# Kernel tuning notes

Measured on AMD Instinct MI355X. Metric: run time of the kernel, lower is better.

Reference implementation:

```python
import jax, jax.numpy as jnp
import numpy as np

B, A, C_CLS = 64, 9, 20
H_FEAT, W_FEAT = 28, 28
IN_DIM, HID = 1280, 128
N_GT, M_POS = 40, 2048
AC5 = 5 * A + C_CLS


def setup_inputs() -> dict:
    key = jax.random.key(0)
    ks = jax.random.split(key, 10)
    features = jax.random.normal(ks[0], (B, IN_DIM, H_FEAT, W_FEAT), jnp.float32)
    # valid GT boxes in feature-map coordinates: (x1, y1, x2, y2, class)
    x1 = jax.random.uniform(ks[1], (B, N_GT), minval=0.0, maxval=W_FEAT - 6.0)
    y1 = jax.random.uniform(ks[2], (B, N_GT), minval=0.0, maxval=H_FEAT - 6.0)
    bw = jax.random.uniform(ks[3], (B, N_GT), minval=1.0, maxval=5.0)
    bh = jax.random.uniform(ks[4], (B, N_GT), minval=1.0, maxval=5.0)
    cls = jax.random.randint(ks[5], (B, N_GT), 0, C_CLS).astype(jnp.float32)
    bboxes = jnp.stack([x1, y1, x1 + bw, y1 + bh, cls], axis=-1)
    n_anchors_total = B * A * H_FEAT * W_FEAT
    pos_anchor_idx = jax.random.randint(ks[6], (M_POS,), 0, n_anchors_total, dtype=jnp.int32)
    neg_anchor_idx = jax.random.randint(ks[7], (M_POS,), 0, n_anchors_total, dtype=jnp.int32)
    W1 = jax.random.normal(ks[8], (HID, IN_DIM), jnp.float32) * 0.02
    b1 = jnp.zeros((HID,), jnp.float32)
    W2 = jax.random.normal(ks[9], (AC5, HID), jnp.float32) * 0.02
    b2 = jnp.zeros((AC5,), jnp.float32)
    anc = jnp.array([[1.0, 1], [2, 2], [3, 3], [4, 4], [5, 5], [2, 3], [3, 2], [3, 5], [5, 3]], jnp.float32)
    return dict(features=features, bboxes=bboxes, pos_anchor_idx=pos_anchor_idx,
                neg_anchor_idx=neg_anchor_idx, W1=W1, b1=b1, W2=W2, b2=b2, anc=anc)


def _detector_loss(features, bboxes, pos_idx, neg_idx, W1, b1, W2, b2, anc):
    Bx, _, Hf, Wf = features.shape
    N = bboxes.shape[1]
    Mp = pos_idx.shape[0]
    # ---- prediction network: two 1x1 convs (dropout skipped: eval mode) ----
    h = jnp.einsum('bchw,oc->bohw', features, W1) + b1[None, :, None, None]
    h = jax.nn.leaky_relu(h, 0.01)
    x = jnp.einsum('bchw,oc->bohw', h, W2) + b2[None, :, None, None]
    x_anchor = x[:, :5 * A].reshape(Bx, A, 5, Hf, Wf)  # (B,A,5,H,W)
    x_class = x[:, 5 * A:]                              # (B,C,H,W)
    # ---- GenerateGrid + GenerateAnchor ----
    xs = jnp.arange(Wf, dtype=jnp.float32) + 0.5
    ys = jnp.arange(Hf, dtype=jnp.float32) + 0.5
    gx, gy = jnp.meshgrid(xs, ys, indexing='xy')        # both (H,W)
    grid = jnp.stack([gx, gy], axis=-1)                 # (H,W,2)
    half = anc / 2.0                                    # (A,2)
    tl = grid[None] - half[:, None, None]               # (A,H,W,2)
    br = grid[None] + half[:, None, None]
    anchors = jnp.concatenate([tl, br], axis=-1)        # (A,H,W,4)
    p = jnp.broadcast_to(anchors[None], (Bx, A, Hf, Wf, 4)).reshape(Bx, -1, 4)  # (B,M,4)
    # ---- IoU matrix (B, M, N), exactly as source (signed w*h -> positive area) ----
    area_p = ((p[..., 0] - p[..., 2]) * (p[..., 1] - p[..., 3]))[:, :, None]
    area_b = ((bboxes[..., 2] - bboxes[..., 0]) * (bboxes[..., 3] - bboxes[..., 1]))[:, None, :]
    ix1 = jnp.maximum(p[:, :, None, 0], bboxes[:, None, :, 0])
    iy1 = jnp.maximum(p[:, :, None, 1], bboxes[:, None, :, 1])
    ix2 = jnp.minimum(p[:, :, None, 2], bboxes[:, None, :, 2])
    iy2 = jnp.minimum(p[:, :, None, 3], bboxes[:, None, :, 3])
    inter = jnp.clip(ix2 - ix1, 0.0) * jnp.clip(iy2 - iy1, 0.0)
    iou_mat = inter / (area_p + area_b - inter)          # (B,M,N)
    # ---- gather-based anchor/class extraction ----
    anc_data = jnp.transpose(x_anchor, (0, 1, 3, 4, 2)).reshape(-1, 5)  # (B*A*H*W, 5)
    pos_a = anc_data[pos_idx]
    neg_a = anc_data[neg_idx]
    conf_scores = jax.nn.sigmoid(jnp.concatenate([pos_a[:, 0], neg_a[:, 0]])[:, None])  # (2M,1)
    off = pos_a[:, 1:]
    offsets = jnp.concatenate([jax.nn.sigmoid(off[:, :2]) - 0.5, off[:, 2:]], axis=1)   # (M,4)
    cls_all = jnp.transpose(x_class, (0, 2, 3, 1))                       # (B,H,W,C)
    cls_all = jnp.broadcast_to(cls_all[:, None], (Bx, A, Hf, Wf, C_CLS)).reshape(-1, C_CLS)
    class_scores = cls_all[pos_idx]                                      # (M,C)
    # ---- match positives to GT via IoU argmax, build GT offsets/classes ----
    Mflat = A * Hf * Wf
    bpos = pos_idx // Mflat
    mpos = pos_idx % Mflat
    iou_pos = iou_mat[bpos, mpos]                 # (M,N)
    matched = jnp.argmax(iou_pos, axis=1)         # (M,)
    gt_box = bboxes[bpos, matched]                # (M,5)
    a_box = p[bpos, mpos]                         # (M,4)
    xa = 0.5 * (a_box[:, 0] + a_box[:, 2]); ya = 0.5 * (a_box[:, 1] + a_box[:, 3])
    wa = a_box[:, 2] - a_box[:, 0];          ha = a_box[:, 3] - a_box[:, 1]
    xb = 0.5 * (gt_box[:, 0] + gt_box[:, 2]); yb = 0.5 * (gt_box[:, 1] + gt_box[:, 3])
    wb = gt_box[:, 2] - gt_box[:, 0];          hb = gt_box[:, 3] - gt_box[:, 1]
    gt_offsets = jnp.stack([xb - xa, yb - ya, jnp.log(wb / wa), jnp.log(hb / ha)], axis=1)
    gt_offsets = jax.lax.stop_gradient(gt_offsets)
    gt_cls = gt_box[:, 4].astype(jnp.int32)
    # ---- losses (w_conf = w_reg = w_cls = 1) ----
    gt_conf = jnp.concatenate([jnp.ones((Mp, 1), jnp.float32), jnp.zeros((Mp, 1), jnp.float32)], axis=0)
    conf_loss = jnp.sum((conf_scores - gt_conf) ** 2) / (2.0 * Mp)
    reg_loss = jnp.sum((offsets - gt_offsets) ** 2) / Mp
    logp = jax.nn.log_softmax(class_scores, axis=-1)
    cls_loss = -jnp.mean(jnp.take_along_axis(logp, gt_cls[:, None], axis=1))
    return conf_loss + reg_loss + cls_loss


def reference(features, bboxes, pos_anchor_idx, neg_anchor_idx, W1, b1, W2, b2, anc):
    return _detector_loss(features, bboxes, pos_anchor_idx, neg_anchor_idx, W1, b1, W2, b2, anc)
```

## Files before the change

kernel.cpp:

```cpp
#include <hip/hip_runtime.h>
#include <math.h>

#define NPOS   2048
#define NANCH  4096
#define CIN    1280
#define HID    128
#define W_     28
#define HW_    784
#define AHW    7056
#define FB     (CIN*HW_)
#define SLAB   4
#define SLABF  (SLAB*HW_)

__device__ __forceinline__ float sigmoidf_(float x) {
    return 1.0f / (1.0f + __expf(-x));
}
__device__ __forceinline__ unsigned short f2bf(float x) {
    unsigned int u = __float_as_uint(x);
    return (unsigned short)((u + 0x7fffu + ((u >> 16) & 1u)) >> 16);
}
__device__ __forceinline__ float bf_lo(unsigned int w) { return __uint_as_float(w << 16); }
__device__ __forceinline__ float bf_hi(unsigned int w) { return __uint_as_float(w & 0xffff0000u); }

typedef __attribute__((address_space(3))) float lds_f;
typedef __attribute__((address_space(1))) const float glb_f;
__device__ __forceinline__ void gload16(const float* g, float* l) {
    __builtin_amdgcn_global_load_lds((glb_f*)g, (lds_f*)l, 16, 0, 0);
}

#define SCHED_FENCE() __builtin_amdgcn_sched_barrier(0)
#define WAIT_VM4()  asm volatile("s_waitcnt vmcnt(4)" ::: "memory")
#define WAIT_VM3()  asm volatile("s_waitcnt vmcnt(3)" ::: "memory")
#define WAIT_VM0()  asm volatile("s_waitcnt vmcnt(0)" ::: "memory")
#define WAIT_LGKM0() asm volatile("s_waitcnt lgkmcnt(0)" ::: "memory")

__global__ __launch_bounds__(256, 4) void k_fused(
    const float* __restrict__ F, const float* __restrict__ W1,
    const int* __restrict__ posi, const int* __restrict__ negi,
    unsigned short* __restrict__ Hp, int kchunk, int nslab)
{
    __shared__ float Pl[2][SLABF];
    __shared__ float Wl[2][520];
    __shared__ int   pkl[128];
    __shared__ int   nbL;

    const int b    = blockIdx.x;
    const int ks   = blockIdx.y;
    const int t    = threadIdx.x;
    const int w    = t >> 6;
    const int lane = t & 63;

    if (t == 0) nbL = 0;
    if (t < 128) pkl[t] = 0;
    __syncthreads();

    const int kb0 = ks * kchunk;

    auto issue = [&](int sl2, int buf) {
        const int kb = kb0 + sl2 * SLAB;
        const float* srcP = F + (size_t)b * FB + (size_t)kb * HW_;
        float* dstP = &Pl[buf][0];
#pragma unroll
        for (int i = 0; i < 3; ++i) {
            const int c = w + 4 * i;
            gload16(srcP + c * 256 + lane * 4, dstP + c * 256);
        }
        if (w == 3) {
            if (lane < 16) gload16(srcP + 3072 + lane * 4, dstP + 3072);
        }
        if (w == 1) gload16(W1 + (size_t)lane * CIN + kb, &Wl[buf][0]);
        if (w == 2) gload16(W1 + (size_t)(64 + lane) * CIN + kb, &Wl[buf][260]);
    };

    issue(0, 0);
    issue(1, 1);

#pragma unroll
    for (int r = 0; r < 16; ++r) {
        const int g    = r * 256 + t;
        const int aidx = (g < NPOS) ? posi[g] : negi[g - NPOS];
        const int bb   = aidx / AHW;
        if (bb == b) {
            const int hw   = (aidx - bb * AHW) % HW_;
            const int slot = atomicAdd(&nbL, 1);
            if (slot < 128) pkl[slot] = (g << 10) | hw;
        }
    }
    WAIT_LGKM0();
    SCHED_FENCE();
    __builtin_amdgcn_s_barrier();
    SCHED_FENCE();

    const int  nb   = nbL;
    const bool wact = (w * 32) < nb;
    const int  og   = lane >> 3;
    const int  al   = w * 32 + (lane & 7) * 4;
    int hwr[4], gr[4];
#pragma unroll
    for (int ai = 0; ai < 4; ++ai) {
        const int a  = al + ai;
        const int pk = pkl[a];
        hwr[ai] = pk & 1023;
        gr[ai]  = (a < nb) ? (pk >> 10) : -1;
    }
    const int WB = (og < 4) ? og * 64 : 260 + (og - 4) * 64;

    float acc[4][16];
#pragma unroll
    for (int ai = 0; ai < 4; ++ai)
#pragma unroll
        for (int m = 0; m < 16; ++m) acc[ai][m] = 0.0f;

    if (w == 0) { WAIT_VM3(); } else { WAIT_VM4(); }
    SCHED_FENCE();
    __builtin_amdgcn_s_barrier();
    SCHED_FENCE();

    for (int sl = 0; sl < nslab; ++sl) {
        const int cur = sl & 1;
        if (wact) {
            float ga[4][4];
#pragma unroll
            for (int ai = 0; ai < 4; ++ai)
#pragma unroll
                for (int c = 0; c < 4; ++c)
                    ga[ai][c] = Pl[cur][c * HW_ + hwr[ai]];
#pragma unroll
            for (int m = 0; m < 16; ++m) {
                const float4 wv = *(const float4*)&Wl[cur][WB + 4 * m];
#pragma unroll
                for (int ai = 0; ai < 4; ++ai) {
                    float v = acc[ai][m];
                    v = fmaf(ga[ai][0], wv.x, v);
                    v = fmaf(ga[ai][1], wv.y, v);
                    v = fmaf(ga[ai][2], wv.z, v);
                    v = fmaf(ga[ai][3], wv.w, v);
                    acc[ai][m] = v;
                }
            }
        }
        if (sl + 1 < nslab) {
            WAIT_LGKM0();
            SCHED_FENCE();
            __builtin_amdgcn_s_barrier();
            SCHED_FENCE();
            if (sl + 2 < nslab) {
                issue(sl + 2, cur);
                SCHED_FENCE();
                if (w == 0) { WAIT_VM3(); } else { WAIT_VM4(); }
            } else {
                WAIT_VM0();
            }
            SCHED_FENCE();
            __builtin_amdgcn_s_barrier();
            SCHED_FENCE();
        }
    }

    if (wact) {
#pragma unroll
        for (int ai = 0; ai < 4; ++ai) {
            const int g = gr[ai];
            if (g >= 0) {
                unsigned short* dst =
                    Hp + ((size_t)ks * NANCH + g) * HID + og * 16;
                unsigned u[8];
#pragma unroll
                for (int q = 0; q < 8; ++q)
                    u[q] = (unsigned)f2bf(acc[ai][2 * q]) |
                           ((unsigned)f2bf(acc[ai][2 * q + 1]) << 16);
                *(uint4*)(dst)     = make_uint4(u[0], u[1], u[2], u[3]);
                *(uint4*)(dst + 8) = make_uint4(u[4], u[5], u[6], u[7]);
            }
        }
    }
}

__global__ __launch_bounds__(256) void k_loss(
    const unsigned short* __restrict__ Hp, const float* __restrict__ b1,
    int ksel, const float* __restrict__ W2, const float* __restrict__ b2,
    const int* __restrict__ posi, const int* __restrict__ negi,
    const float* __restrict__ bboxes, const float* __restrict__ anc,
    float* __restrict__ contrib)
{
    const int wid  = threadIdx.x >> 6;
    const int lane = threadIdx.x & 63;
    const int g    = blockIdx.x * 4 + wid;

    const int aidx = (g < NPOS) ? posi[g] : negi[g - NPOS];
    const int b   = aidx / AHW;
    const int rem = aidx - b * AHW;
    const int a   = rem / HW_;
    const int hw  = rem - a * HW_;
    const int hh  = hw / W_;
    const int ww  = hw - hh * W_;

    float hx = b1[2 * lane], hy = b1[2 * lane + 1];
    for (int ks = 0; ks < ksel; ++ks) {
        const unsigned raw =
            *(const unsigned*)&Hp[((size_t)ks * NANCH + g) * HID + 2 * lane];
        hx += bf_lo(raw);
        hy += bf_hi(raw);
    }
    hx = (hx > 0.0f) ? hx : 0.01f * hx;
    hy = (hy > 0.0f) ? hy : 0.01f * hy;

    if (g < NPOS) {
        float outv[25];
#pragma unroll
        for (int j = 0; j < 25; ++j) {
            const int row = (j < 5) ? (5 * a + j) : (40 + j);
            const float2 w = *(const float2*)&W2[(size_t)row * HID + 2 * lane];
            float v = fmaf(w.x, hx, w.y * hy);
#pragma unroll
            for (int off = 1; off < 64; off <<= 1) v += __shfl_xor(v, off, 64);
            outv[j] = v + b2[row];
        }

        const float wa = anc[2 * a], ha = anc[2 * a + 1];
        const float cx = ww + 0.5f, cy = hh + 0.5f;
        const float ax1 = cx - 0.5f * wa, ay1 = cy - 0.5f * ha;
        const float ax2 = cx + 0.5f * wa, ay2 = cy + 0.5f * ha;
        const float areap = wa * ha;

        float v; int vi = lane;
        if (lane < 40) {
            const float* bb = &bboxes[(size_t)(b * 40 + lane) * 5];
            const float bx1 = bb[0], by1 = bb[1], bx2 = bb[2], by2 = bb[3];
            const float areab = (bx2 - bx1) * (by2 - by1);
            const float ix1 = fmaxf(ax1, bx1), iy1 = fmaxf(ay1, by1);
            const float ix2 = fminf(ax2, bx2), iy2 = fminf(ay2, by2);
            const float inter = fmaxf(ix2 - ix1, 0.0f) * fmaxf(iy2 - iy1, 0.0f);
            v = inter / (areap + areab - inter);
        } else {
            v = -1.0f;
        }
#pragma unroll
        for (int off = 1; off < 64; off <<= 1) {
            const float ov = __shfl_xor(v, off, 64);
            const int   oi = __shfl_xor(vi, off, 64);
            if (ov > v || (ov == v && oi < vi)) { v = ov; vi = oi; }
        }
        const int m = vi;

        const float* gt = &bboxes[(size_t)(b * 40 + m) * 5];
        const float gx1 = gt[0], gy1 = gt[1], gx2 = gt[2], gy2 = gt[3];
        const int   gcls = (int)gt[4];
        const float xb = 0.5f * (gx1 + gx2), yb = 0.5f * (gy1 + gy2);
        const float wb = gx2 - gx1, hb = gy2 - gy1;
        const float go0 = xb - cx, go1 = yb - cy;
        const float go2 = __logf(wb / wa), go3 = __logf(hb / ha);

        const float o0 = sigmoidf_(outv[1]) - 0.5f;
        const float o1 = sigmoidf_(outv[2]) - 0.5f;
        const float o2 = outv[3], o3 = outv[4];
        const float reg = (o0 - go0) * (o0 - go0) + (o1 - go1) * (o1 - go1) +
                          (o2 - go2) * (o2 - go2) + (o3 - go3) * (o3 - go3);

        const float conf = sigmoidf_(outv[0]);
        const float conft = (conf - 1.0f) * (conf - 1.0f);

        float mx = outv[5];
#pragma unroll
        for (int c = 1; c < 20; ++c) mx = fmaxf(mx, outv[5 + c]);
        float se = 0.0f;
#pragma unroll
        for (int c = 0; c < 20; ++c) se += __expf(outv[5 + c] - mx);
        float lgt = 0.0f;
#pragma unroll
        for (int c = 0; c < 20; ++c) if (c == gcls) lgt = outv[5 + c];
        const float clst = -(lgt - mx - __logf(se));

        if (lane == 0)
            contrib[g] = conft * (1.0f / 4096.0f) + reg * (1.0f / 2048.0f) +
                         clst * (1.0f / 2048.0f);
    } else {
        const int row = 5 * a;
        const float2 w = *(const float2*)&W2[(size_t)row * HID + 2 * lane];
        float v = fmaf(w.x, hx, w.y * hy);
#pragma unroll
        for (int off = 1; off < 64; off <<= 1) v += __shfl_xor(v, off, 64);
        const float conf = sigmoidf_(v + b2[row]);
        if (lane == 0) contrib[g] = conf * conf * (1.0f / 4096.0f);
    }
}

__global__ __launch_bounds__(256) void k_final(const float* __restrict__ contrib,
                                               float* __restrict__ out)
{
    __shared__ float red[256];
    const int t = threadIdx.x;
    float s = 0.0f;
    for (int i = t; i < NANCH; i += 256) s += contrib[i];
    red[t] = s;
    __syncthreads();
    for (int st = 128; st > 0; st >>= 1) {
        if (t < st) red[t] += red[t + st];
        __syncthreads();
    }
    if (t == 0) out[0] = red[0];
}

extern "C" void kernel_launch(void* const* d_in, const int* in_sizes, int n_in,
                              void* d_out, int out_size, void* d_ws, size_t ws_size,
                              hipStream_t stream)
{
    const float* F      = (const float*)d_in[0];
    const float* bboxes = (const float*)d_in[1];
    const int*   posi   = (const int*)d_in[2];
    const int*   negi   = (const int*)d_in[3];
    const float* W1     = (const float*)d_in[4];
    const float* b1     = (const float*)d_in[5];
    const float* W2     = (const float*)d_in[6];
    const float* b2     = (const float*)d_in[7];
    const float* anc    = (const float*)d_in[8];
    float* out = (float*)d_out;

    char* ws = (char*)d_ws;
    int KSEL = 4;
    {
        const int opts[3] = {16, 8, 4};
        for (int i = 0; i < 3; ++i) {
            size_t need = (size_t)opts[i] * NANCH * HID * 2 + (size_t)NANCH * 4 + 256;
            if (need <= ws_size) { KSEL = opts[i]; break; }
        }
    }
    unsigned short* Hp      = (unsigned short*)ws;
    float*          contrib = (float*)(ws + (size_t)KSEL * NANCH * HID * 2);

    const int kchunk = CIN / KSEL;
    const int nslab  = kchunk / SLAB;

    k_fused<<<dim3(64, KSEL), 256, 0, stream>>>(F, W1, posi, negi, Hp,
                                                kchunk, nslab);
    k_loss<<<NANCH / 4, 256, 0, stream>>>(Hp, b1, KSEL, W2, b2, posi, negi,
                                          bboxes, anc, contrib);
    k_final<<<1, 256, 0, stream>>>(contrib, out);
    (void)in_sizes; (void)n_in; (void)out_size;
}
```

Baseline: 85.23 us.

## Replace LDS-staged slab streaming with direct gathers of needed feature pixels

The first kernel no longer streams whole channel slabs of the feature map into LDS through double-buffered async global-to-LDS loads. Each thread now reads only the feature values at its sampled anchor pixels, plus W1 rows, straight from global memory. Waves with no sampled anchors exit early. This removes reading the full feature map and the barrier-heavy pipeline, but turns the loads into scattered, uncoalesced accesses with no prefetch overlap and repeated W1 reads from every wave.

Result: slower. 126.4 us (+48.3%).

```diff
diff --git a/kernel.cpp b/kernel.cpp
--- a/kernel.cpp
+++ b/kernel.cpp
@@ -9,8 +9,6 @@
 #define HW_    784
 #define AHW    7056
 #define FB     (CIN*HW_)
-#define SLAB   4
-#define SLABF  (SLAB*HW_)
 
 __device__ __forceinline__ float sigmoidf_(float x) {
     return 1.0f / (1.0f + __expf(-x));
@@ -22,27 +20,13 @@
 __device__ __forceinline__ float bf_lo(unsigned int w) { return __uint_as_float(w << 16); }
 __device__ __forceinline__ float bf_hi(unsigned int w) { return __uint_as_float(w & 0xffff0000u); }
 
-typedef __attribute__((address_space(3))) float lds_f;
-typedef __attribute__((address_space(1))) const float glb_f;
-__device__ __forceinline__ void gload16(const float* g, float* l) {
-    __builtin_amdgcn_global_load_lds((glb_f*)g, (lds_f*)l, 16, 0, 0);
-}
-
-#define SCHED_FENCE() __builtin_amdgcn_sched_barrier(0)
-#define WAIT_VM4()  asm volatile("s_waitcnt vmcnt(4)" ::: "memory")
-#define WAIT_VM3()  asm volatile("s_waitcnt vmcnt(3)" ::: "memory")
-#define WAIT_VM0()  asm volatile("s_waitcnt vmcnt(0)" ::: "memory")
-#define WAIT_LGKM0() asm volatile("s_waitcnt lgkmcnt(0)" ::: "memory")
-
-__global__ __launch_bounds__(256, 4) void k_fused(
+__global__ __launch_bounds__(256, 4) void k_main(
     const float* __restrict__ F, const float* __restrict__ W1,
     const int* __restrict__ posi, const int* __restrict__ negi,
-    unsigned short* __restrict__ Hp, int kchunk, int nslab)
-{
-    __shared__ float Pl[2][SLABF];
-    __shared__ float Wl[2][520];
-    __shared__ int   pkl[128];
-    __shared__ int   nbL;
+    unsigned short* __restrict__ Hp, int kchunk, int nsub)
+{
+    __shared__ int pkl[128];
+    __shared__ int nbL;
 
     const int b    = blockIdx.x;
     const int ks   = blockIdx.y;
@@ -53,28 +37,6 @@
     if (t == 0) nbL = 0;
     if (t < 128) pkl[t] = 0;
     __syncthreads();
-
-    const int kb0 = ks * kchunk;
-
-    auto issue = [&](int sl2, int buf) {
-        const int kb = kb0 + sl2 * SLAB;
-        const float* srcP = F + (size_t)b * FB + (size_t)kb * HW_;
-        float* dstP = &Pl[buf][0];
-#pragma unroll
-        for (int i = 0; i < 3; ++i) {
-            const int c = w + 4 * i;
-            gload16(srcP + c * 256 + lane * 4, dstP + c * 256);
-        }
-        if (w == 3) {
-            if (lane < 16) gload16(srcP + 3072 + lane * 4, dstP + 3072);
-        }
-        if (w == 1) gload16(W1 + (size_t)lane * CIN + kb, &Wl[buf][0]);
-        if (w == 2) gload16(W1 + (size_t)(64 + lane) * CIN + kb, &Wl[buf][260]);
-    };
-
-    issue(0, 0);
-    issue(1, 1);
-
 #pragma unroll
     for (int r = 0; r < 16; ++r) {
         const int g    = r * 256 + t;
@@ -86,15 +48,14 @@
             if (slot < 128) pkl[slot] = (g << 10) | hw;
         }
     }
-    WAIT_LGKM0();
-    SCHED_FENCE();
-    __builtin_amdgcn_s_barrier();
-    SCHED_FENCE();
-
-    const int  nb   = nbL;
+    __syncthreads();
+    const int nb = nbL;
+
     const bool wact = (w * 32) < nb;
-    const int  og   = lane >> 3;
-    const int  al   = w * 32 + (lane & 7) * 4;
+    if (!wact) return;
+
+    const int og = lane >> 3;
+    const int al = w * 32 + (lane & 7) * 4;
     int hwr[4], gr[4];
 #pragma unroll
     for (int ai = 0; ai < 4; ++ai) {
@@ -103,7 +64,13 @@
         hwr[ai] = pk & 1023;
         gr[ai]  = (a < nb) ? (pk >> 10) : -1;
     }
-    const int WB = (og < 4) ? og * 64 : 260 + (og - 4) * 64;
+
+    const int kb0 = ks * kchunk;
+    const float* fa0 = F + (size_t)b * FB + (size_t)kb0 * HW_ + hwr[0];
+    const float* fa1 = F + (size_t)b * FB + (size_t)kb0 * HW_ + hwr[1];
+    const float* fa2 = F + (size_t)b * FB + (size_t)kb0 * HW_ + hwr[2];
+    const float* fa3 = F + (size_t)b * FB + (size_t)kb0 * HW_ + hwr[3];
+    const float* Wb  = W1 + (size_t)(og * 16) * CIN + kb0;
 
     float acc[4][16];
 #pragma unroll
@@ -111,67 +78,43 @@
 #pragma unroll
         for (int m = 0; m < 16; ++m) acc[ai][m] = 0.0f;
 
-    if (w == 0) { WAIT_VM3(); } else { WAIT_VM4(); }
-    SCHED_FENCE();
-    __builtin_amdgcn_s_barrier();
-    SCHED_FENCE();
-
-    for (int sl = 0; sl < nslab; ++sl) {
-        const int cur = sl & 1;
-        if (wact) {
-            float ga[4][4];
-#pragma unroll
-            for (int ai = 0; ai < 4; ++ai)
-#pragma unroll
-                for (int c = 0; c < 4; ++c)
-                    ga[ai][c] = Pl[cur][c * HW_ + hwr[ai]];
-#pragma unroll
-            for (int m = 0; m < 16; ++m) {
-                const float4 wv = *(const float4*)&Wl[cur][WB + 4 * m];
-#pragma unroll
-                for (int ai = 0; ai < 4; ++ai) {
-                    float v = acc[ai][m];
-                    v = fmaf(ga[ai][0], wv.x, v);
-                    v = fmaf(ga[ai][1], wv.y, v);
-                    v = fmaf(ga[ai][2], wv.z, v);
-                    v = fmaf(ga[ai][3], wv.w, v);
-                    acc[ai][m] = v;
-                }
+    for (int s = 0; s < nsub; ++s) {
+        float ga[4][4];
+#pragma unroll
+        for (int c = 0; c < 4; ++c) {
+            const size_t off = (size_t)(4 * s + c) * HW_;
+            ga[0][c] = fa0[off];
+            ga[1][c] = fa1[off];
+            ga[2][c] = fa2[off];
+            ga[3][c] = fa3[off];
+        }
+#pragma unroll
+        for (int m = 0; m < 16; ++m) {
+            const float4 wv = *(const float4*)&Wb[(size_t)m * CIN + 4 * s];
+#pragma unroll
+            for (int ai = 0; ai < 4; ++ai) {
+                float v = acc[ai][m];
+                v = fmaf(ga[ai][0], wv.x, v);
+                v = fmaf(ga[ai][1], wv.y, v);
+                v = fmaf(ga[ai][2], wv.z, v);
+                v = fmaf(ga[ai][3], wv.w, v);
+                acc[ai][m] = v;
             }
         }
-        if (sl + 1 < nslab) {
-            WAIT_LGKM0();
-            SCHED_FENCE();
-            __builtin_amdgcn_s_barrier();
-            SCHED_FENCE();
-            if (sl + 2 < nslab) {
-                issue(sl + 2, cur);
-                SCHED_FENCE();
-                if (w == 0) { WAIT_VM3(); } else { WAIT_VM4(); }
-            } else {
-                WAIT_VM0();
-            }
-            SCHED_FENCE();
-            __builtin_amdgcn_s_barrier();
-            SCHED_FENCE();
-        }
-    }
-
-    if (wact) {
-#pragma unroll
-        for (int ai = 0; ai < 4; ++ai) {
-            const int g = gr[ai];
-            if (g >= 0) {
-                unsigned short* dst =
-                    Hp + ((size_t)ks * NANCH + g) * HID + og * 16;
-                unsigned u[8];
-#pragma unroll
-                for (int q = 0; q < 8; ++q)
-                    u[q] = (unsigned)f2bf(acc[ai][2 * q]) |
-                           ((unsigned)f2bf(acc[ai][2 * q + 1]) << 16);
-                *(uint4*)(dst)     = make_uint4(u[0], u[1], u[2], u[3]);
-                *(uint4*)(dst + 8) = make_uint4(u[4], u[5], u[6], u[7]);
-            }
+    }
+
+#pragma unroll
+    for (int ai = 0; ai < 4; ++ai) {
+        const int g = gr[ai];
+        if (g >= 0) {
+            unsigned short* dst = Hp + ((size_t)ks * NANCH + g) * HID + og * 16;
+            unsigned u[8];
+#pragma unroll
+            for (int q = 0; q < 8; ++q)
+                u[q] = (unsigned)f2bf(acc[ai][2 * q]) |
+                       ((unsigned)f2bf(acc[ai][2 * q + 1]) << 16);
+            *(uint4*)(dst)     = make_uint4(u[0], u[1], u[2], u[3]);
+            *(uint4*)(dst + 8) = make_uint4(u[4], u[5], u[6], u[7]);
         }
     }
 }
@@ -329,10 +272,10 @@
     float*          contrib = (float*)(ws + (size_t)KSEL * NANCH * HID * 2);
 
     const int kchunk = CIN / KSEL;
-    const int nslab  = kchunk / SLAB;
-
-    k_fused<<<dim3(64, KSEL), 256, 0, stream>>>(F, W1, posi, negi, Hp,
-                                                kchunk, nslab);
+    const int nsub   = kchunk / 4;
+
+    k_main<<<dim3(64, KSEL), 256, 0, stream>>>(F, W1, posi, negi, Hp,
+                                               kchunk, nsub);
     k_loss<<<NANCH / 4, 256, 0, stream>>>(Hp, b1, KSEL, W2, b2, posi, negi,
                                           bboxes, anc, contrib);
     k_final<<<1, 256, 0, stream>>>(contrib, out);
```

## Preload W1 chunk into LDS once and hardcode KSEL=16 split

Applied to the files above, without the earlier changes.

Each block now loads its whole W1 k-chunk (80 channels x 128 outputs) into a resident, padded LDS array up front through registers, instead of streaming a W1 slice with every feature slab. The streaming pipeline then moves only feature data. KSEL is fixed at compile time to 16, so loops unroll and the runtime workspace-size check is dropped, and launch bounds go from 4 to 2 blocks per CU. The larger LDS footprint lowers occupancy, and the workspace is assumed large enough for 16 partials.

After: 106.0 us. 24.4% more time.

```diff
diff --git a/kernel.cpp b/kernel.cpp
--- a/kernel.cpp
+++ b/kernel.cpp
@@ -11,6 +11,9 @@
 #define FB     (CIN*HW_)
 #define SLAB   4
 #define SLABF  (SLAB*HW_)
+#define KSEL   16
+#define KCH    (CIN/KSEL)
+#define NSLAB  (KCH/SLAB)
 
 __device__ __forceinline__ float sigmoidf_(float x) {
     return 1.0f / (1.0f + __expf(-x));
@@ -34,13 +37,13 @@
 #define WAIT_VM0()  asm volatile("s_waitcnt vmcnt(0)" ::: "memory")
 #define WAIT_LGKM0() asm volatile("s_waitcnt lgkmcnt(0)" ::: "memory")
 
-__global__ __launch_bounds__(256, 4) void k_fused(
+__global__ __launch_bounds__(256, 2) void k_fused(
     const float* __restrict__ F, const float* __restrict__ W1,
     const int* __restrict__ posi, const int* __restrict__ negi,
-    unsigned short* __restrict__ Hp, int kchunk, int nslab)
+    unsigned short* __restrict__ Hp)
 {
     __shared__ float Pl[2][SLABF];
-    __shared__ float Wl[2][520];
+    __shared__ float Wres[NSLAB * 544];
     __shared__ int   pkl[128];
     __shared__ int   nbL;
 
@@ -49,31 +52,22 @@
     const int t    = threadIdx.x;
     const int w    = t >> 6;
     const int lane = t & 63;
+    const int kb0  = ks * KCH;
 
     if (t == 0) nbL = 0;
     if (t < 128) pkl[t] = 0;
     __syncthreads();
 
-    const int kb0 = ks * kchunk;
-
-    auto issue = [&](int sl2, int buf) {
-        const int kb = kb0 + sl2 * SLAB;
-        const float* srcP = F + (size_t)b * FB + (size_t)kb * HW_;
-        float* dstP = &Pl[buf][0];
-#pragma unroll
-        for (int i = 0; i < 3; ++i) {
-            const int c = w + 4 * i;
-            gload16(srcP + c * 256 + lane * 4, dstP + c * 256);
-        }
-        if (w == 3) {
-            if (lane < 16) gload16(srcP + 3072 + lane * 4, dstP + 3072);
-        }
-        if (w == 1) gload16(W1 + (size_t)lane * CIN + kb, &Wl[buf][0]);
-        if (w == 2) gload16(W1 + (size_t)(64 + lane) * CIN + kb, &Wl[buf][260]);
-    };
-
-    issue(0, 0);
-    issue(1, 1);
+    float4 wreg[10];
+    const int o_w  = t & 127;
+    const int grp  = t >> 7;
+    const int og_w = o_w >> 4;
+    const int m_w  = o_w & 15;
+#pragma unroll
+    for (int j0 = 0; j0 < 10; ++j0) {
+        const int j = grp * 10 + j0;
+        wreg[j0] = *(const float4*)&W1[(size_t)o_w * CIN + kb0 + 4 * j];
+    }
 
 #pragma unroll
     for (int r = 0; r < 16; ++r) {
@@ -86,15 +80,19 @@
             if (slot < 128) pkl[slot] = (g << 10) | hw;
         }
     }
-    WAIT_LGKM0();
-    SCHED_FENCE();
-    __builtin_amdgcn_s_barrier();
-    SCHED_FENCE();
-
-    const int  nb   = nbL;
+    __syncthreads();
+
+#pragma unroll
+    for (int j0 = 0; j0 < 10; ++j0) {
+        const int j = grp * 10 + j0;
+        *(float4*)&Wres[j * 544 + og_w * 68 + m_w * 4] = wreg[j0];
+    }
+    __syncthreads();
+
+    const int nb = nbL;
     const bool wact = (w * 32) < nb;
-    const int  og   = lane >> 3;
-    const int  al   = w * 32 + (lane & 7) * 4;
+    const int  og = lane >> 3;
+    const int  al = w * 32 + (lane & 7) * 4;
     int hwr[4], gr[4];
 #pragma unroll
     for (int ai = 0; ai < 4; ++ai) {
@@ -103,7 +101,6 @@
         hwr[ai] = pk & 1023;
         gr[ai]  = (a < nb) ? (pk >> 10) : -1;
     }
-    const int WB = (og < 4) ? og * 64 : 260 + (og - 4) * 64;
 
     float acc[4][16];
 #pragma unroll
@@ -111,12 +108,27 @@
 #pragma unroll
         for (int m = 0; m < 16; ++m) acc[ai][m] = 0.0f;
 
-    if (w == 0) { WAIT_VM3(); } else { WAIT_VM4(); }
+    auto issue = [&](int sl2, int buf) {
+        const float* srcP = F + (size_t)b * FB + (size_t)(kb0 + sl2 * SLAB) * HW_;
+        float* dstP = &Pl[buf][0];
+#pragma unroll
+        for (int i = 0; i < 3; ++i) {
+            const int c = w + 4 * i;
+            gload16(srcP + c * 256 + lane * 4, dstP + c * 256);
+        }
+        if (w == 3 && lane < 16)
+            gload16(srcP + 3072 + lane * 4, dstP + 3072);
+    };
+
+    issue(0, 0);
+    issue(1, 1);
+    SCHED_FENCE();
+    if (w == 3) { WAIT_VM4(); } else { WAIT_VM3(); }
     SCHED_FENCE();
     __builtin_amdgcn_s_barrier();
     SCHED_FENCE();
 
-    for (int sl = 0; sl < nslab; ++sl) {
+    for (int sl = 0; sl < NSLAB; ++sl) {
         const int cur = sl & 1;
         if (wact) {
             float ga[4][4];
@@ -125,9 +137,10 @@
 #pragma unroll
                 for (int c = 0; c < 4; ++c)
                     ga[ai][c] = Pl[cur][c * HW_ + hwr[ai]];
+            const float* wb = &Wres[sl * 544 + og * 68];
 #pragma unroll
             for (int m = 0; m < 16; ++m) {
-                const float4 wv = *(const float4*)&Wl[cur][WB + 4 * m];
+                const float4 wv = *(const float4*)&wb[4 * m];
 #pragma unroll
                 for (int ai = 0; ai < 4; ++ai) {
                     float v = acc[ai][m];
@@ -139,15 +152,15 @@
                 }
             }
         }
-        if (sl + 1 < nslab) {
+        if (sl + 1 < NSLAB) {
             WAIT_LGKM0();
             SCHED_FENCE();
             __builtin_amdgcn_s_barrier();
             SCHED_FENCE();
-            if (sl + 2 < nslab) {
+            if (sl + 2 < NSLAB) {
                 issue(sl + 2, cur);
                 SCHED_FENCE();
-                if (w == 0) { WAIT_VM3(); } else { WAIT_VM4(); }
+                if (w == 3) { WAIT_VM4(); } else { WAIT_VM3(); }
             } else {
                 WAIT_VM0();
             }
@@ -178,7 +191,7 @@
 
 __global__ __launch_bounds__(256) void k_loss(
     const unsigned short* __restrict__ Hp, const float* __restrict__ b1,
-    int ksel, const float* __restrict__ W2, const float* __restrict__ b2,
+    const float* __restrict__ W2, const float* __restrict__ b2,
     const int* __restrict__ posi, const int* __restrict__ negi,
     const float* __restrict__ bboxes, const float* __restrict__ anc,
     float* __restrict__ contrib)
@@ -196,7 +209,8 @@
     const int ww  = hw - hh * W_;
 
     float hx = b1[2 * lane], hy = b1[2 * lane + 1];
-    for (int ks = 0; ks < ksel; ++ks) {
+#pragma unroll
+    for (int ks = 0; ks < KSEL; ++ks) {
         const unsigned raw =
             *(const unsigned*)&Hp[((size_t)ks * NANCH + g) * HID + 2 * lane];
         hx += bf_lo(raw);
@@ -317,24 +331,12 @@
     float* out = (float*)d_out;
 
     char* ws = (char*)d_ws;
-    int KSEL = 4;
-    {
-        const int opts[3] = {16, 8, 4};
-        for (int i = 0; i < 3; ++i) {
-            size_t need = (size_t)opts[i] * NANCH * HID * 2 + (size_t)NANCH * 4 + 256;
-            if (need <= ws_size) { KSEL = opts[i]; break; }
-        }
-    }
     unsigned short* Hp      = (unsigned short*)ws;
     float*          contrib = (float*)(ws + (size_t)KSEL * NANCH * HID * 2);
 
-    const int kchunk = CIN / KSEL;
-    const int nslab  = kchunk / SLAB;
-
-    k_fused<<<dim3(64, KSEL), 256, 0, stream>>>(F, W1, posi, negi, Hp,
-                                                kchunk, nslab);
-    k_loss<<<NANCH / 4, 256, 0, stream>>>(Hp, b1, KSEL, W2, b2, posi, negi,
+    k_fused<<<dim3(64, KSEL), 256, 0, stream>>>(F, W1, posi, negi, Hp);
+    k_loss<<<NANCH / 4, 256, 0, stream>>>(Hp, b1, W2, b2, posi, negi,
                                           bboxes, anc, contrib);
     k_final<<<1, 256, 0, stream>>>(contrib, out);
-    (void)in_sizes; (void)n_in; (void)out_size;
-}
+    (void)in_sizes; (void)n_in; (void)out_size; (void)ws_size;
+}
```
